# Optimization experiments

Hardware: AMD Instinct MI355X
Metric: run time of the kernel (lower is better)

The kernel has to match this reference:

```python
import jax, jax.numpy as jnp
from jax import lax
import numpy as np

T, INPUT, RES, OUT = 4096, 64, 4096, 32
SPECTRAL_RADIUS, CONNECTIVITY = 0.9, 0.3


def setup_inputs() -> dict:
    key = jax.random.key(0)
    k_in, k_w, k_mask, k_x, k_out = jax.random.split(key, 5)
    inputs = jax.random.normal(k_x, (T, INPUT), dtype=jnp.float32)
    # W_in, W ~ U(-1, 1), as in (rand - 0.5) * 2
    W_in = jax.random.uniform(k_in, (RES, INPUT), minval=-1.0, maxval=1.0, dtype=jnp.float32)
    W = jax.random.uniform(k_w, (RES, RES), minval=-1.0, maxval=1.0, dtype=jnp.float32)
    mask = (jax.random.uniform(k_mask, (RES, RES)) < CONNECTIVITY).astype(jnp.float32)
    W = W * mask
    # rescale to spectral radius (done once at init; numpy eig on host)
    max_eig = np.max(np.abs(np.linalg.eigvals(np.asarray(W))))
    W = W / jnp.float32(max_eig / SPECTRAL_RADIUS)
    # trained readout (stand-in for pinv-solved W_out)
    W_out = jax.random.normal(k_out, (RES, OUT), dtype=jnp.float32) * 0.05
    return {"inputs": inputs, "W_in": W_in, "W": W, "W_out": W_out}


def reference(inputs, W_in, W, W_out):
    # X[:, 0] = 0; X[:, t] = tanh(W_in @ inputs[t] + W @ X[:, t-1]) for t >= 1
    u = inputs @ W_in.T  # [T, RES] precomputed input projections

    def step(x_prev, u_t):
        x_t = jnp.tanh(u_t + W @ x_prev)
        return x_t, x_t

    x0 = jnp.zeros((RES,), dtype=inputs.dtype)
    _, xs = lax.scan(step, x0, u[1:])  # [T-1, RES]
    X = jnp.concatenate([x0[None, :], xs], axis=0)  # [T, RES] == original X.T
    return X @ W_out  # [T, OUT]
```

## Files before the change

### kernel.cpp

```cpp
#include <hip/hip_runtime.h>
#include <hip/hip_fp16.h>

#define T_STEPS 4096
#define RES     4096
#define NIN     64
#define NOUT    32
#define NWG     256
#define TPB     512
#define WS      4168
#define WR      (WS / 8)

typedef unsigned long long ull;
typedef _Float16 hv2 __attribute__((ext_vector_type(2)));

__device__ __forceinline__ float dot8(uint4 wq, uint4 xq, float acc) {
    acc = __builtin_amdgcn_fdot2(__builtin_bit_cast(hv2, wq.x), __builtin_bit_cast(hv2, xq.x), acc, false);
    acc = __builtin_amdgcn_fdot2(__builtin_bit_cast(hv2, wq.y), __builtin_bit_cast(hv2, xq.y), acc, false);
    acc = __builtin_amdgcn_fdot2(__builtin_bit_cast(hv2, wq.z), __builtin_bit_cast(hv2, xq.z), acc, false);
    acc = __builtin_amdgcn_fdot2(__builtin_bit_cast(hv2, wq.w), __builtin_bit_cast(hv2, xq.w), acc, false);
    return acc;
}

__device__ __forceinline__ bool ok4(ull q) {
    return ((unsigned short)q) && ((unsigned short)(q >> 16)) &&
           ((unsigned short)(q >> 32)) && ((unsigned short)(q >> 48));
}

__device__ __forceinline__ unsigned sub2(unsigned u) {
    __half2 h = *(__half2*)&u;
    __half2 r = __hsub2(h, __floats2half2_rn(2.f, 2.f));
    return *(unsigned*)&r;
}

__global__ void esn_init(unsigned short* __restrict__ Xh) {
    int i = blockIdx.x * 256 + threadIdx.x;
    if (i < RES) Xh[i] = 0x4000;
}

__global__ __launch_bounds__(TPB, 1)
void esn_recur(const float* __restrict__ inp,
               const float* __restrict__ Win,
               const float* __restrict__ W,
               unsigned short* __restrict__ Xh)
{
    __shared__ __align__(16) __half Wl[16 * WS];
    __shared__ __align__(16) __half xh[RES + NIN];
    __shared__ float red[2][16][33];

    const int g    = blockIdx.x;
    const int tid  = threadIdx.x;
    const int wv   = tid >> 6;
    const int lane = tid & 63;
    const int r    = lane & 15;
    const int cg   = lane >> 4;

    {
        const float4* Wg = (const float4*)(W + (size_t)g * 16 * RES);
        for (int idx = tid; idx < 16 * RES / 4; idx += TPB) {
            float4 v  = Wg[idx];
            int  row  = idx >> 10;
            int  c    = (idx & 1023) * 4;
            __half* d = &Wl[row * WS + c];
            d[0] = __float2half_rn(v.x);
            d[1] = __float2half_rn(v.y);
            d[2] = __float2half_rn(v.z);
            d[3] = __float2half_rn(v.w);
        }
        for (int idx = tid; idx < 16 * NIN; idx += TPB) {
            int row = idx >> 6, k = idx & 63;
            Wl[row * WS + RES + k] = __float2half_rn(Win[(size_t)(g * 16 + row) * NIN + k]);
        }
    }

    float u_cur = (wv == 0) ? inp[NIN + lane] : 0.f;

    __syncthreads();

    const uint4* WQ    = (const uint4*)Wl;
    const uint4* XQ    = (const uint4*)xh;
    const int    wbase = r * WR + wv * 64 + 16 * cg;
    const int    xbase = wv * 64 + 16 * cg;

    for (int t = 1; t < T_STEPS; ++t) {
        uint4 wq[16];
#pragma unroll
        for (int i = 0; i < 16; ++i)
            wq[i] = WQ[wbase + ((i + 4 * cg) & 15)];
        uint4 wu0, wu1;
        if (wv == 0) {
            wu0 = WQ[r * WR + 512 + 2 * cg];
            wu1 = WQ[r * WR + 513 + 2 * cg];
        }
        asm volatile("s_waitcnt lgkmcnt(0)" ::: "memory");

        const ull* src = (const ull*)(Xh + (size_t)(t - 1) * RES) + 128 * wv + 2 * lane;
        ull q0 = 0, q1 = 0;
        int need = 3;
        do {
            if (need & 1) { q0 = __hip_atomic_load(src,     __ATOMIC_RELAXED, __HIP_MEMORY_SCOPE_AGENT); if (ok4(q0)) need &= ~1; }
            if (need & 2) { q1 = __hip_atomic_load(src + 1, __ATOMIC_RELAXED, __HIP_MEMORY_SCOPE_AGENT); if (ok4(q1)) need &= ~2; }
        } while (need);

        uint4 sv;
        sv.x = sub2((unsigned)q0); sv.y = sub2((unsigned)(q0 >> 32));
        sv.z = sub2((unsigned)q1); sv.w = sub2((unsigned)(q1 >> 32));
        *(uint4*)(xh + 512 * wv + 8 * lane) = sv;
        if (wv == 0) xh[RES + lane] = __float2half_rn(u_cur);
        asm volatile("s_waitcnt lgkmcnt(0)" ::: "memory");

        float acc = 0.f;
#pragma unroll
        for (int i = 0; i < 16; ++i) {
            uint4 xq = XQ[xbase + ((i + 4 * cg) & 15)];
            acc = dot8(wq[i], xq, acc);
        }
        if (wv == 0) {
            const uint4* XU = (const uint4*)(xh + RES);
            acc = dot8(wu0, XU[2 * cg], acc);
            acc = dot8(wu1, XU[2 * cg + 1], acc);
            u_cur = (t + 1 < T_STEPS) ? inp[(size_t)(t + 1) * NIN + lane] : 0.f;
        }
        red[t & 1][r][4 * wv + cg] = acc;
        __syncthreads();

        {
            const int row = 2 * wv + (lane >> 5);
            float s = red[t & 1][row][lane & 31];
            s += __shfl_xor(s, 1, 64);
            s += __shfl_xor(s, 2, 64);
            s += __shfl_xor(s, 4, 64);
            s += __shfl_xor(s, 8, 64);
            s += __shfl_xor(s, 16, 64);
            float xn = tanhf(s);
            unsigned enc = (unsigned)__half_as_ushort(__float2half_rn(xn + 2.0f));
            unsigned hi  = (unsigned)__shfl((int)enc, 32, 64);
            if (lane == 0) {
                unsigned pk = enc | (hi << 16);
                __hip_atomic_store((unsigned*)(Xh + (size_t)t * RES + 16 * g + 2 * wv), pk,
                                   __ATOMIC_RELAXED, __HIP_MEMORY_SCOPE_AGENT);
            }
        }
    }
}

__global__ __launch_bounds__(256)
void esn_out(const unsigned short* __restrict__ Xh,
             const float* __restrict__ Wout,
             float* __restrict__ out)
{
    __shared__ float xs[2 * RES];
    __shared__ float red[2][8][32];
    const int tid = threadIdx.x;
    const int t0  = blockIdx.x * 2;

    const uint4* s4 = (const uint4*)(Xh + (size_t)t0 * RES);
    for (int i = tid; i < 2 * RES / 8; i += 256) {
        uint4 v  = s4[i];
        float* d = &xs[8 * i];
        float2 f;
        f = __half22float2(*(__half2*)&v.x); d[0] = f.x - 2.f; d[1] = f.y - 2.f;
        f = __half22float2(*(__half2*)&v.y); d[2] = f.x - 2.f; d[3] = f.y - 2.f;
        f = __half22float2(*(__half2*)&v.z); d[4] = f.x - 2.f; d[5] = f.y - 2.f;
        f = __half22float2(*(__half2*)&v.w); d[6] = f.x - 2.f; d[7] = f.y - 2.f;
    }
    __syncthreads();

    const int o  = tid & 31;
    const int sg = tid >> 5;
    float acc0 = 0.f, acc1 = 0.f;
    const int rbeg = sg * 512;
    for (int rr = rbeg; rr < rbeg + 512; ++rr) {
        float wv = Wout[(size_t)rr * NOUT + o];
        acc0 += xs[rr] * wv;
        acc1 += xs[RES + rr] * wv;
    }
    red[0][sg][o] = acc0;
    red[1][sg][o] = acc1;
    __syncthreads();

    if (tid < 64) {
        const int h = tid >> 5, oo = tid & 31;
        float s = 0.f;
#pragma unroll
        for (int k = 0; k < 8; ++k) s += red[h][k][oo];
        out[(size_t)(t0 + h) * NOUT + oo] = s;
    }
}

extern "C" void kernel_launch(void* const* d_in, const int* in_sizes, int n_in,
                              void* d_out, int out_size, void* d_ws, size_t ws_size,
                              hipStream_t stream)
{
    const float* inputs = (const float*)d_in[0];
    const float* W_in   = (const float*)d_in[1];
    const float* W      = (const float*)d_in[2];
    const float* W_out  = (const float*)d_in[3];
    float* out = (float*)d_out;

    unsigned short* Xh = (unsigned short*)d_ws;

    hipMemsetAsync(Xh, 0, (size_t)T_STEPS * RES * sizeof(unsigned short), stream);
    esn_init<<<dim3((RES + 255) / 256), dim3(256), 0, stream>>>(Xh);

    esn_recur<<<dim3(NWG), dim3(TPB), 0, stream>>>(inputs, W_in, W, Xh);
    esn_out<<<dim3(T_STEPS / 2), dim3(256), 0, stream>>>(Xh, W_out, out);
}
```

Measured before the change: 11.86 ms.

## Use MFMA with register-resident W slices and bias-corrected offset encoding

Replaces the per-step LDS weight reads and fdot2 dot products with 16x16x32 f16 MFMA instructions on W slices held in registers for the whole recurrence. The +2 offset is no longer removed from the loaded state; instead each row's weight sum times 2 is precomputed once and subtracted after accumulation. Input projection is computed each step directly from global inputs with MFMA. This drops the shared-memory W copy and per-step LDS bandwidth, but MFMA on a single column wastes most of the matrix unit and adds register pressure. Subtracting the large offset term in fp32 may also cost precision.

```diff
diff --git a/kernel.cpp b/kernel.cpp
--- a/kernel.cpp
+++ b/kernel.cpp
@@ -7,29 +7,14 @@
 #define NOUT    32
 #define NWG     256
 #define TPB     512
-#define WS      4168
-#define WR      (WS / 8)
 
 typedef unsigned long long ull;
-typedef _Float16 hv2 __attribute__((ext_vector_type(2)));
-
-__device__ __forceinline__ float dot8(uint4 wq, uint4 xq, float acc) {
-    acc = __builtin_amdgcn_fdot2(__builtin_bit_cast(hv2, wq.x), __builtin_bit_cast(hv2, xq.x), acc, false);
-    acc = __builtin_amdgcn_fdot2(__builtin_bit_cast(hv2, wq.y), __builtin_bit_cast(hv2, xq.y), acc, false);
-    acc = __builtin_amdgcn_fdot2(__builtin_bit_cast(hv2, wq.z), __builtin_bit_cast(hv2, xq.z), acc, false);
-    acc = __builtin_amdgcn_fdot2(__builtin_bit_cast(hv2, wq.w), __builtin_bit_cast(hv2, xq.w), acc, false);
-    return acc;
-}
+typedef _Float16 half8 __attribute__((ext_vector_type(8)));
+typedef float    f32x4 __attribute__((ext_vector_type(4)));
 
 __device__ __forceinline__ bool ok4(ull q) {
     return ((unsigned short)q) && ((unsigned short)(q >> 16)) &&
            ((unsigned short)(q >> 32)) && ((unsigned short)(q >> 48));
-}
-
-__device__ __forceinline__ unsigned sub2(unsigned u) {
-    __half2 h = *(__half2*)&u;
-    __half2 r = __hsub2(h, __floats2half2_rn(2.f, 2.f));
-    return *(unsigned*)&r;
 }
 
 __global__ void esn_init(unsigned short* __restrict__ Xh) {
@@ -43,56 +28,61 @@
                const float* __restrict__ W,
                unsigned short* __restrict__ Xh)
 {
-    __shared__ __align__(16) __half Wl[16 * WS];
-    __shared__ __align__(16) __half xh[RES + NIN];
-    __shared__ float red[2][16][33];
+    __shared__ __align__(16) __half xh[RES];
+    __shared__ float red[2][16][9];
 
     const int g    = blockIdx.x;
     const int tid  = threadIdx.x;
     const int wv   = tid >> 6;
     const int lane = tid & 63;
     const int r    = lane & 15;
-    const int cg   = lane >> 4;
-
+    const int q    = lane >> 4;
+
+    half8 wA[16];
     {
-        const float4* Wg = (const float4*)(W + (size_t)g * 16 * RES);
-        for (int idx = tid; idx < 16 * RES / 4; idx += TPB) {
-            float4 v  = Wg[idx];
-            int  row  = idx >> 10;
-            int  c    = (idx & 1023) * 4;
-            __half* d = &Wl[row * WS + c];
-            d[0] = __float2half_rn(v.x);
-            d[1] = __float2half_rn(v.y);
-            d[2] = __float2half_rn(v.z);
-            d[3] = __float2half_rn(v.w);
-        }
-        for (int idx = tid; idx < 16 * NIN; idx += TPB) {
-            int row = idx >> 6, k = idx & 63;
-            Wl[row * WS + RES + k] = __float2half_rn(Win[(size_t)(g * 16 + row) * NIN + k]);
-        }
-    }
-
-    float u_cur = (wv == 0) ? inp[NIN + lane] : 0.f;
-
-    __syncthreads();
-
-    const uint4* WQ    = (const uint4*)Wl;
-    const uint4* XQ    = (const uint4*)xh;
-    const int    wbase = r * WR + wv * 64 + 16 * cg;
-    const int    xbase = wv * 64 + 16 * cg;
+        const float* base = W + (size_t)(g * 16 + r) * RES + wv * 512 + 8 * q;
+#pragma unroll
+        for (int c = 0; c < 16; ++c) {
+            float4 a = *(const float4*)(base + 32 * c);
+            float4 b = *(const float4*)(base + 32 * c + 4);
+            half8 f;
+            f[0] = (_Float16)a.x; f[1] = (_Float16)a.y;
+            f[2] = (_Float16)a.z; f[3] = (_Float16)a.w;
+            f[4] = (_Float16)b.x; f[5] = (_Float16)b.y;
+            f[6] = (_Float16)b.z; f[7] = (_Float16)b.w;
+            wA[c] = f;
+        }
+    }
+    half8 wI0, wI1;
+    if (wv == 0) {
+        const float* base = Win + (size_t)(g * 16 + r) * NIN + 8 * q;
+#pragma unroll
+        for (int cu = 0; cu < 2; ++cu) {
+            float4 a = *(const float4*)(base + 32 * cu);
+            float4 b = *(const float4*)(base + 32 * cu + 4);
+            half8 f;
+            f[0] = (_Float16)a.x; f[1] = (_Float16)a.y;
+            f[2] = (_Float16)a.z; f[3] = (_Float16)a.w;
+            f[4] = (_Float16)b.x; f[5] = (_Float16)b.y;
+            f[6] = (_Float16)b.z; f[7] = (_Float16)b.w;
+            if (cu == 0) wI0 = f; else wI1 = f;
+        }
+    }
+    f32x4 rs;
+    {
+        half8 ones;
+#pragma unroll
+        for (int j = 0; j < 8; ++j) ones[j] = (_Float16)1.0f;
+        f32x4 s0 = {0.f, 0.f, 0.f, 0.f}, s1 = {0.f, 0.f, 0.f, 0.f};
+#pragma unroll
+        for (int c = 0; c < 16; c += 2) {
+            s0 = __builtin_amdgcn_mfma_f32_16x16x32_f16(wA[c],     ones, s0, 0, 0, 0);
+            s1 = __builtin_amdgcn_mfma_f32_16x16x32_f16(wA[c + 1], ones, s1, 0, 0, 0);
+        }
+        rs = (s0 + s1) * 2.0f;
+    }
 
     for (int t = 1; t < T_STEPS; ++t) {
-        uint4 wq[16];
-#pragma unroll
-        for (int i = 0; i < 16; ++i)
-            wq[i] = WQ[wbase + ((i + 4 * cg) & 15)];
-        uint4 wu0, wu1;
-        if (wv == 0) {
-            wu0 = WQ[r * WR + 512 + 2 * cg];
-            wu1 = WQ[r * WR + 513 + 2 * cg];
-        }
-        asm volatile("s_waitcnt lgkmcnt(0)" ::: "memory");
-
         const ull* src = (const ull*)(Xh + (size_t)(t - 1) * RES) + 128 * wv + 2 * lane;
         ull q0 = 0, q1 = 0;
         int need = 3;
@@ -102,41 +92,56 @@
         } while (need);
 
         uint4 sv;
-        sv.x = sub2((unsigned)q0); sv.y = sub2((unsigned)(q0 >> 32));
-        sv.z = sub2((unsigned)q1); sv.w = sub2((unsigned)(q1 >> 32));
+        sv.x = (unsigned)q0; sv.y = (unsigned)(q0 >> 32);
+        sv.z = (unsigned)q1; sv.w = (unsigned)(q1 >> 32);
         *(uint4*)(xh + 512 * wv + 8 * lane) = sv;
-        if (wv == 0) xh[RES + lane] = __float2half_rn(u_cur);
         asm volatile("s_waitcnt lgkmcnt(0)" ::: "memory");
 
-        float acc = 0.f;
-#pragma unroll
-        for (int i = 0; i < 16; ++i) {
-            uint4 xq = XQ[xbase + ((i + 4 * cg) & 15)];
-            acc = dot8(wq[i], xq, acc);
+        const half8* xb = (const half8*)(xh + 512 * wv + 8 * q);
+        f32x4 acc0 = {0.f, 0.f, 0.f, 0.f}, acc1 = {0.f, 0.f, 0.f, 0.f};
+#pragma unroll
+        for (int c = 0; c < 16; c += 2) {
+            acc0 = __builtin_amdgcn_mfma_f32_16x16x32_f16(wA[c],     xb[4 * c],       acc0, 0, 0, 0);
+            acc1 = __builtin_amdgcn_mfma_f32_16x16x32_f16(wA[c + 1], xb[4 * (c + 1)], acc1, 0, 0, 0);
         }
         if (wv == 0) {
-            const uint4* XU = (const uint4*)(xh + RES);
-            acc = dot8(wu0, XU[2 * cg], acc);
-            acc = dot8(wu1, XU[2 * cg + 1], acc);
-            u_cur = (t + 1 < T_STEPS) ? inp[(size_t)(t + 1) * NIN + lane] : 0.f;
-        }
-        red[t & 1][r][4 * wv + cg] = acc;
+            const float* up = inp + (size_t)t * NIN + 8 * q;
+            float4 ua = *(const float4*)up,        ub = *(const float4*)(up + 4);
+            float4 uc = *(const float4*)(up + 32), ud = *(const float4*)(up + 36);
+            half8 b0, b1;
+            b0[0] = (_Float16)ua.x; b0[1] = (_Float16)ua.y;
+            b0[2] = (_Float16)ua.z; b0[3] = (_Float16)ua.w;
+            b0[4] = (_Float16)ub.x; b0[5] = (_Float16)ub.y;
+            b0[6] = (_Float16)ub.z; b0[7] = (_Float16)ub.w;
+            b1[0] = (_Float16)uc.x; b1[1] = (_Float16)uc.y;
+            b1[2] = (_Float16)uc.z; b1[3] = (_Float16)uc.w;
+            b1[4] = (_Float16)ud.x; b1[5] = (_Float16)ud.y;
+            b1[6] = (_Float16)ud.z; b1[7] = (_Float16)ud.w;
+            acc0 = __builtin_amdgcn_mfma_f32_16x16x32_f16(wI0, b0, acc0, 0, 0, 0);
+            acc1 = __builtin_amdgcn_mfma_f32_16x16x32_f16(wI1, b1, acc1, 0, 0, 0);
+        }
+        f32x4 acc = acc0 + acc1;
+
+        if ((lane & 15) == 0) {
+#pragma unroll
+            for (int i = 0; i < 4; ++i)
+                red[t & 1][4 * q + i][wv] = acc[i] - rs[i];
+        }
         __syncthreads();
 
         {
-            const int row = 2 * wv + (lane >> 5);
-            float s = red[t & 1][row][lane & 31];
+            const int row = 2 * wv + ((lane >> 3) & 1);
+            float s = red[t & 1][row][lane & 7];
             s += __shfl_xor(s, 1, 64);
             s += __shfl_xor(s, 2, 64);
             s += __shfl_xor(s, 4, 64);
-            s += __shfl_xor(s, 8, 64);
-            s += __shfl_xor(s, 16, 64);
-            float xn = tanhf(s);
-            unsigned enc = (unsigned)__half_as_ushort(__float2half_rn(xn + 2.0f));
-            unsigned hi  = (unsigned)__shfl((int)enc, 32, 64);
+            float s2 = __shfl_xor(s, 8, 64);
             if (lane == 0) {
-                unsigned pk = enc | (hi << 16);
-                __hip_atomic_store((unsigned*)(Xh + (size_t)t * RES + 16 * g + 2 * wv), pk,
+                float x0 = tanhf(s), x1 = tanhf(s2);
+                unsigned e0 = (unsigned)__half_as_ushort(__float2half_rn(x0 + 2.0f));
+                unsigned e1 = (unsigned)__half_as_ushort(__float2half_rn(x1 + 2.0f));
+                __hip_atomic_store((unsigned*)(Xh + (size_t)t * RES + 16 * g) + wv,
+                                   e0 | (e1 << 16),
                                    __ATOMIC_RELAXED, __HIP_MEMORY_SCOPE_AGENT);
             }
         }
```

New measurement: 22.39 ms. 88.8% more time.
